# Performance work log

Hardware: AMD Instinct MI355X
Metric: run time of the kernel (lower is better)

The kernel has to match this reference:

```python
import jax, jax.numpy as jnp
import numpy as np

EMBED_DIM = 512
NUM_HEADS = 8
HEAD_DIM = EMBED_DIM // NUM_HEADS
EDGE_DIM = 16
B, N = 2, 2048


def setup_inputs() -> dict:
    key = jax.random.key(0)
    ks = jax.random.split(key, 16)
    s = 1.0 / np.sqrt(EMBED_DIM)
    inp = {
        "x": jax.random.normal(ks[0], (B, N, EMBED_DIM), dtype=jnp.float32),
        "adjacency": jax.random.uniform(ks[1], (B, N, N), dtype=jnp.float32),
        # torch.nn.Linear stores weight as (out, in); we keep that convention
        "Wq": jax.random.uniform(ks[2], (EMBED_DIM, EMBED_DIM), minval=-s, maxval=s),
        "bq": jax.random.uniform(ks[3], (EMBED_DIM,), minval=-s, maxval=s),
        "Wk": jax.random.uniform(ks[4], (EMBED_DIM, EMBED_DIM), minval=-s, maxval=s),
        "bk": jax.random.uniform(ks[5], (EMBED_DIM,), minval=-s, maxval=s),
        "Wv": jax.random.uniform(ks[6], (EMBED_DIM, EMBED_DIM), minval=-s, maxval=s),
        "bv": jax.random.uniform(ks[7], (EMBED_DIM,), minval=-s, maxval=s),
        "Wo": jax.random.uniform(ks[8], (EMBED_DIM, EMBED_DIM), minval=-s, maxval=s),
        "bo": jax.random.uniform(ks[9], (EMBED_DIM,), minval=-s, maxval=s),
        # edge MLP: Linear(1 -> edge_dim) then Linear(edge_dim -> num_heads)
        "We1": jax.random.uniform(ks[10], (EDGE_DIM, 1), minval=-1.0, maxval=1.0),
        "be1": jax.random.uniform(ks[11], (EDGE_DIM,), minval=-1.0, maxval=1.0),
        "We2": jax.random.uniform(ks[12], (NUM_HEADS, EDGE_DIM), minval=-0.25, maxval=0.25),
        "be2": jax.random.uniform(ks[13], (NUM_HEADS,), minval=-0.25, maxval=0.25),
        "edge_bias": jnp.zeros((NUM_HEADS,), dtype=jnp.float32),
    }
    return inp


def reference(x, adjacency, Wq, bq, Wk, bk, Wv, bv, Wo, bo, We1, be1, We2, be2, edge_bias):
    b, n, _ = x.shape
    scale = HEAD_DIM ** (-0.5)

    def split_heads(t):  # (b, n, E) -> (b, H, n, d)
        return t.reshape(b, n, NUM_HEADS, HEAD_DIM).transpose(0, 2, 1, 3)

    q = split_heads(x @ Wq.T + bq)
    k = split_heads(x @ Wk.T + bk)
    v = split_heads(x @ Wv.T + bv)

    # (b, H, n, n)
    attn_scores = jnp.einsum('bhid,bhjd->bhij', q, k) * scale

    # edge MLP applied pointwise to each adjacency entry: 1 -> edge_dim -> num_heads
    # hidden: (b, n, n, edge_dim)
    hidden = jax.nn.relu(adjacency[..., None] * We1[:, 0] + be1)
    edge_attn = jnp.einsum('bijE,hE->bhij', hidden, We2) + be2[None, :, None, None]

    boost = adjacency[:, None, :, :] * edge_bias[None, :, None, None]
    attn_scores = attn_scores + edge_attn + boost

    attn_probs = jax.nn.softmax(attn_scores, axis=-1)
    out = jnp.einsum('bhij,bhjd->bhid', attn_probs, v)
    out = out.transpose(0, 2, 1, 3).reshape(b, n, EMBED_DIM)
    out = out @ Wo.T + bo
    return out
```

## Files before the change

kernel.cpp:

```cpp
#include <hip/hip_runtime.h>
#include <stdint.h>


#define SEQ 2048
#define EMB 512
#define NH  8
#define HD  64
#define NB  2

typedef unsigned int   u32;
typedef unsigned short u16;
typedef u32   u32x4  __attribute__((ext_vector_type(4)));
typedef float f32x4  __attribute__((ext_vector_type(4)));
typedef __bf16 bf16x8 __attribute__((ext_vector_type(8)));

#define MFMA16(a, b, c) __builtin_amdgcn_mfma_f32_16x16x32_bf16((a), (b), (c), 0, 0, 0)

static __device__ __forceinline__ u16 f2bf(float f) {
  u32 u = __builtin_bit_cast(u32, f);
  return (u16)((u + 0x7fffu + ((u >> 16) & 1u)) >> 16);
}
static __device__ __forceinline__ bf16x8 ldfrag(const u16* p) {
  return __builtin_bit_cast(bf16x8, *(const u32x4*)p);
}

__global__ void cvt_bf16_kernel(const float* __restrict__ s, u16* __restrict__ d, int n) {
  int i = (blockIdx.x * blockDim.x + threadIdx.x) * 4;
  if (i >= n) return;
  float4 v = *(const float4*)(s + i);
  u32 lo = (u32)f2bf(v.x) | ((u32)f2bf(v.y) << 16);
  u32 hi = (u32)f2bf(v.z) | ((u32)f2bf(v.w) << 16);
  *(uint2*)(d + i) = make_uint2(lo, hi);
}

__global__ void cvt_w_kernel(const float* __restrict__ Wq, const float* __restrict__ Wk,
                             const float* __restrict__ Wv, const float* __restrict__ Wo,
                             u16* __restrict__ wqkv, u16* __restrict__ wob) {
  int i = (blockIdx.x * blockDim.x + threadIdx.x) * 4;
  int m = i >> 18;
  int off = i & 262143;
  const float* src = (m == 0) ? Wq : ((m == 1) ? Wk : ((m == 2) ? Wv : Wo));
  u16* dst = (m < 3) ? (wqkv + (size_t)m * 262144) : wob;
  float4 v = *(const float4*)(src + off);
  u32 lo = (u32)f2bf(v.x) | ((u32)f2bf(v.y) << 16);
  u32 hi = (u32)f2bf(v.z) | ((u32)f2bf(v.w) << 16);
  *(uint2*)(dst + off) = make_uint2(lo, hi);
}

__global__ void edge_coeff_kernel(const float* __restrict__ We1, const float* __restrict__ be1,
                                  const float* __restrict__ We2, const float* __restrict__ be2,
                                  const float* __restrict__ ebias, float* __restrict__ co) {
  const int t = threadIdx.x;
  const int e = t & 15, h = t >> 4;
  float w1 = We1[e], b1 = be1[e], w2 = We2[h * 16 + e];
  float u0 = b1, u1 = w1 + b1;
  bool on  = (u0 >= 0.0f) && (u1 >= 0.0f);
  bool off = (u0 <= 0.0f) && (u1 <= 0.0f);
  bool crossing = (!on) && (!off);
  float ca = on ? (w2 * b1) : (crossing ? 0.5f * w2 * b1 : 0.0f);
  float cb = on ? (w2 * w1) : (crossing ? 0.5f * w2 * w1 : 0.0f);
  #pragma unroll
  for (int d = 1; d < 16; d <<= 1) {
    ca += __shfl_xor(ca, d);
    cb += __shfl_xor(cb, d);
  }
  if (e == 0) { co[h] = be2[h] + ca; co[8 + h] = ebias[h] + cb; }
  unsigned long long msk = __ballot(crossing);
  int midx = __popcll(msk & 0xFFFFull & ((1ull << e) - 1ull));
  int mcnt = __popcll(msk & 0xFFFFull);
  if (crossing) {
    co[49 + midx * 8 + h] = 0.5f * w2;
    if (h == 0 || h == 4) {  }
    if (h == 0) { co[17 + midx] = w1; co[33 + midx] = b1; }
  }
  if (t == 0) ((int*)co)[16] = mcnt;
}

#define LDA 40
__global__ __launch_bounds__(256) void gemm_qkv_kernel(
    const u16* __restrict__ A, const u16* __restrict__ Bm,
    const float* __restrict__ bq, const float* __restrict__ bk, const float* __restrict__ bv,
    u16* __restrict__ qh, u16* __restrict__ kh, u16* __restrict__ vh)
{
  __shared__ u16 As[128 * LDA];
  __shared__ u16 Bs[128 * LDA];
  const int tid = threadIdx.x;
  const int lane = tid & 63, wid = tid >> 6;
  const int q = lane >> 4, l15 = lane & 15;
  const int m0 = blockIdx.y * 128;
  const int n0 = blockIdx.x * 128;
  const int wh = wid >> 1, ww = wid & 1;

  f32x4 acc[4][4];
  f32x4 zero = {0.f, 0.f, 0.f, 0.f};
  #pragma unroll
  for (int i = 0; i < 4; i++)
    #pragma unroll
    for (int j = 0; j < 4; j++) acc[i][j] = zero;

  const int srow = tid >> 1, shalf = tid & 1;
  const u16* ga = A  + (size_t)(m0 + srow) * EMB + shalf * 16;
  const u16* gb = Bm + (size_t)(n0 + srow) * EMB + shalf * 16;
  u16* la = &As[srow * LDA + shalf * 16];
  u16* lb = &Bs[srow * LDA + shalf * 16];

  u32x4 pa0 = *(const u32x4*)(ga);
  u32x4 pa1 = *(const u32x4*)(ga + 8);
  u32x4 pb0 = *(const u32x4*)(gb);
  u32x4 pb1 = *(const u32x4*)(gb + 8);
  ga += 32; gb += 32;

  for (int k0 = 0; k0 < EMB; k0 += 32) {
    __syncthreads();
    *(u32x4*)(la)     = pa0; *(u32x4*)(la + 8) = pa1;
    *(u32x4*)(lb)     = pb0; *(u32x4*)(lb + 8) = pb1;
    __syncthreads();
    if (k0 + 32 < EMB) {
      pa0 = *(const u32x4*)(ga);
      pa1 = *(const u32x4*)(ga + 8);
      pb0 = *(const u32x4*)(gb);
      pb1 = *(const u32x4*)(gb + 8);
      ga += 32; gb += 32;
    }
    bf16x8 af[4], bfr[4];
    #pragma unroll
    for (int mi = 0; mi < 4; mi++)
      af[mi] = ldfrag(&As[(wh*64 + mi*16 + l15) * LDA + q*8]);
    #pragma unroll
    for (int ni = 0; ni < 4; ni++)
      bfr[ni] = ldfrag(&Bs[(ww*64 + ni*16 + l15) * LDA + q*8]);
    #pragma unroll
    for (int mi = 0; mi < 4; mi++)
      #pragma unroll
      for (int ni = 0; ni < 4; ni++)
        acc[mi][ni] = MFMA16(af[mi], bfr[ni], acc[mi][ni]);
  }

  const int mat = n0 >> 9;
  const float* bias = (mat == 0) ? bq : ((mat == 1) ? bk : bv);
  u16* dst = (mat == 0) ? qh : ((mat == 1) ? kh : vh);
  const float mul = (mat == 0) ? 0.125f : 1.0f;

  #pragma unroll
  for (int mi = 0; mi < 4; mi++) {
    int rowb = m0 + wh*64 + mi*16 + q*4;
    #pragma unroll
    for (int ni = 0; ni < 4; ni++) {
      int col = n0 + ww*64 + ni*16 + l15;
      int oo = col & 511;
      float bsv = bias[oo];
      int h = oo >> 6, dd = oo & 63;
      #pragma unroll
      for (int r = 0; r < 4; r++) {
        int grow = rowb + r;
        int b_ = grow >> 11, n_ = grow & 2047;
        float val = (acc[mi][ni][r] + bsv) * mul;
        dst[((size_t)(b_ * NH + h) * SEQ + n_) * HD + dd] = f2bf(val);
      }
    }
  }
}

__global__ __launch_bounds__(256) void gemm_out_kernel(
    const u16* __restrict__ A, const u16* __restrict__ Bm,
    const float* __restrict__ bo, float* __restrict__ out)
{
  __shared__ u16 As[64 * LDA];
  __shared__ u16 Bs[128 * LDA];
  const int tid = threadIdx.x;
  const int lane = tid & 63, w = tid >> 6;
  const int q = lane >> 4, l15 = lane & 15;
  const int m0 = blockIdx.y * 64;
  const int n0 = blockIdx.x * 128;

  f32x4 acc[4][2];
  f32x4 zero = {0.f, 0.f, 0.f, 0.f};
  #pragma unroll
  for (int i = 0; i < 4; i++) { acc[i][0] = zero; acc[i][1] = zero; }

  const bool isA = tid < 128;
  const int arow = tid >> 1, ahalf = tid & 1;
  const int brow = tid - 128;
  const u16* ga = A  + (size_t)(m0 + arow) * EMB + ahalf * 16;
  const u16* gb = Bm + (size_t)(n0 + brow) * EMB;
  u16* la = &As[arow * LDA + ahalf * 16];
  u16* lb = &Bs[brow * LDA];

  u32x4 p0, p1, p2, p3;
  if (isA) {
    p0 = *(const u32x4*)(ga);
    p1 = *(const u32x4*)(ga + 8);
    ga += 32;
  } else {
    p0 = *(const u32x4*)(gb);
    p1 = *(const u32x4*)(gb + 8);
    p2 = *(const u32x4*)(gb + 16);
    p3 = *(const u32x4*)(gb + 24);
    gb += 32;
  }

  for (int k0 = 0; k0 < EMB; k0 += 32) {
    __syncthreads();
    if (isA) {
      *(u32x4*)(la)     = p0; *(u32x4*)(la + 8) = p1;
    } else {
      *(u32x4*)(lb)      = p0; *(u32x4*)(lb + 8)  = p1;
      *(u32x4*)(lb + 16) = p2; *(u32x4*)(lb + 24) = p3;
    }
    __syncthreads();
    if (k0 + 32 < EMB) {
      if (isA) {
        p0 = *(const u32x4*)(ga);
        p1 = *(const u32x4*)(ga + 8);
        ga += 32;
      } else {
        p0 = *(const u32x4*)(gb);
        p1 = *(const u32x4*)(gb + 8);
        p2 = *(const u32x4*)(gb + 16);
        p3 = *(const u32x4*)(gb + 24);
        gb += 32;
      }
    }
    bf16x8 af[4], bfr[2];
    #pragma unroll
    for (int mi = 0; mi < 4; mi++)
      af[mi] = ldfrag(&As[(mi*16 + l15) * LDA + q*8]);
    #pragma unroll
    for (int ni = 0; ni < 2; ni++)
      bfr[ni] = ldfrag(&Bs[(w*32 + ni*16 + l15) * LDA + q*8]);
    #pragma unroll
    for (int mi = 0; mi < 4; mi++)
      #pragma unroll
      for (int ni = 0; ni < 2; ni++)
        acc[mi][ni] = MFMA16(af[mi], bfr[ni], acc[mi][ni]);
  }

  #pragma unroll
  for (int mi = 0; mi < 4; mi++) {
    int rowb = m0 + mi*16 + q*4;
    #pragma unroll
    for (int ni = 0; ni < 2; ni++) {
      int col = n0 + w*32 + ni*16 + l15;
      float bsv = bo[col];
      #pragma unroll
      for (int r = 0; r < 4; r++)
        out[(size_t)(rowb + r) * EMB + col] = acc[mi][ni][r] + bsv;
    }
  }
}

__global__ __launch_bounds__(256) void vtrans_kernel(const u16* __restrict__ vh, u16* __restrict__ vt) {
  __shared__ u16 Ts[64 * 72];
  const int b = blockIdx.z, h = blockIdx.y, j0 = blockIdx.x * 64;
  const int t = threadIdx.x;
  const u16* src = vh + ((size_t)(b * NH + h) * SEQ + j0) * HD;
  {
    int r = t >> 2, c = t & 3;
    *(u32x4*)&Ts[r*72 + c*16]     = *(const u32x4*)(src + r*HD + c*16);
    *(u32x4*)&Ts[r*72 + c*16 + 8] = *(const u32x4*)(src + r*HD + c*16 + 8);
  }
  __syncthreads();
  int d = t >> 2, jc = t & 3;
  u32 wv[8];
  #pragma unroll
  for (int p = 0; p < 8; p++) {
    u32 lo = Ts[(jc*16 + 2*p    ) * 72 + d];
    u32 hi = Ts[(jc*16 + 2*p + 1) * 72 + d];
    wv[p] = lo | (hi << 16);
  }
  u16* dst = vt + ((size_t)(b * NH + h) * HD + d) * SEQ + j0 + jc * 16;
  u32x4 w0 = {wv[0], wv[1], wv[2], wv[3]};
  u32x4 w1 = {wv[4], wv[5], wv[6], wv[7]};
  *(u32x4*)(dst)     = w0;
  *(u32x4*)(dst + 8) = w1;
}

__global__ __launch_bounds__(256) void flash_kernel(
    const u16* __restrict__ qh, const u16* __restrict__ kh, const u16* __restrict__ vt,
    const float* __restrict__ adj, const float* __restrict__ coeff, u16* __restrict__ om)
{
  __shared__ u16 Ks[64 * 72];
  __shared__ u16 Vs[64 * 72];
  __shared__ u16 Ps[4 * 16 * 72];

  const int tid = threadIdx.x, lane = tid & 63, w = tid >> 6;
  const int q = lane >> 4, l15 = lane & 15;
  const int i0 = blockIdx.x * 64;
  const int h = blockIdx.y, b = blockIdx.z;
  const int bh = b * NH + h;

  const float Ah = coeff[h], Bh = coeff[8 + h];
  const int mterms = ((const int*)coeff)[16];

  const u16* qbase = qh + ((size_t)bh * SEQ + i0 + w*16 + l15) * HD + q*8;
  bf16x8 qf0 = ldfrag(qbase);
  bf16x8 qf1 = ldfrag(qbase + 32);

  f32x4 O[4];
  f32x4 zero = {0.f, 0.f, 0.f, 0.f};
  #pragma unroll
  for (int dt = 0; dt < 4; dt++) O[dt] = zero;
  float lsum[4] = {0.f, 0.f, 0.f, 0.f};

  const u16* kgbase = kh + (size_t)bh * SEQ * HD;
  const u16* vgbase = vt + (size_t)bh * HD * SEQ;
  const float* abase = adj + ((size_t)b * SEQ + i0 + w*16 + q*4) * SEQ;

  const int sr = tid >> 2, sc = tid & 3;
  u16* psw = &Ps[w * 16 * 72];

  u32x4 pk0, pk1, pv0, pv1;
  float padj[16];
  {
    const u16* gk = kgbase + (size_t)sr * HD + sc * 16;
    const u16* gv = vgbase + (size_t)sr * SEQ + sc * 16;
    pk0 = *(const u32x4*)(gk);
    pk1 = *(const u32x4*)(gk + 8);
    pv0 = *(const u32x4*)(gv);
    pv1 = *(const u32x4*)(gv + 8);
    #pragma unroll
    for (int jt = 0; jt < 4; jt++)
      #pragma unroll
      for (int r = 0; r < 4; r++)
        padj[jt*4 + r] = abase[(size_t)r * SEQ + jt*16 + l15];
  }

  for (int it = 0; it < 32; it++) {
    __syncthreads();
    *(u32x4*)&Ks[sr*72 + sc*16]     = pk0;
    *(u32x4*)&Ks[sr*72 + sc*16 + 8] = pk1;
    *(u32x4*)&Vs[sr*72 + sc*16]     = pv0;
    *(u32x4*)&Vs[sr*72 + sc*16 + 8] = pv1;
    __syncthreads();

    const int nx = (it + 1 < 32) ? (it + 1) * 64 : 0;

    {
      const u16* gk = kgbase + (size_t)(nx + sr) * HD + sc * 16;
      const u16* gv = vgbase + (size_t)sr * SEQ + nx + sc * 16;
      pk0 = *(const u32x4*)(gk);
      pk1 = *(const u32x4*)(gk + 8);
      pv0 = *(const u32x4*)(gv);
      pv1 = *(const u32x4*)(gv + 8);
    }

    float eb[16];
    #pragma unroll
    for (int jt = 0; jt < 4; jt++)
      #pragma unroll
      for (int r = 0; r < 4; r++)
        eb[jt*4 + r] = fmaf(padj[jt*4 + r], Bh, Ah);
    for (int t = 0; t < mterms; t++) {
      float ct = coeff[17 + t], dt_ = coeff[33 + t], wt = coeff[49 + t*8 + h];
      #pragma unroll
      for (int jt = 0; jt < 4; jt++)
        #pragma unroll
        for (int r = 0; r < 4; r++)
          eb[jt*4 + r] = fmaf(fabsf(fmaf(padj[jt*4 + r], ct, dt_)), wt, eb[jt*4 + r]);
    }

    #pragma unroll
    for (int jt = 0; jt < 4; jt++)
      #pragma unroll
      for (int r = 0; r < 4; r++)
        padj[jt*4 + r] = abase[(size_t)r * SEQ + nx + jt*16 + l15];

    f32x4 S[4];
    #pragma unroll
    for (int jt = 0; jt < 4; jt++) {
      bf16x8 kf0 = ldfrag(&Ks[(jt*16 + l15) * 72 + q*8]);
      bf16x8 kf1 = ldfrag(&Ks[(jt*16 + l15) * 72 + 32 + q*8]);
      f32x4 s = zero;
      s = MFMA16(qf0, kf0, s);
      s = MFMA16(qf1, kf1, s);
      S[jt] = s;
    }

    #pragma unroll
    for (int jt = 0; jt < 4; jt++) {
      #pragma unroll
      for (int r = 0; r < 4; r++) {
        float p = __expf(S[jt][r] + eb[jt*4 + r]);
        lsum[r] += p;
        psw[(q*4 + r) * 72 + jt*16 + l15] = f2bf(p);
      }
    }

    bf16x8 pf0 = ldfrag(&psw[l15 * 72 + q*8]);
    bf16x8 pf1 = ldfrag(&psw[l15 * 72 + 32 + q*8]);
    #pragma unroll
    for (int dt = 0; dt < 4; dt++) {
      bf16x8 vf0 = ldfrag(&Vs[(dt*16 + l15) * 72 + q*8]);
      bf16x8 vf1 = ldfrag(&Vs[(dt*16 + l15) * 72 + 32 + q*8]);
      O[dt] = MFMA16(pf0, vf0, O[dt]);
      O[dt] = MFMA16(pf1, vf1, O[dt]);
    }
  }

  float rl[4];
  #pragma unroll
  for (int r = 0; r < 4; r++) {
    float v = lsum[r];
    v += __shfl_xor(v, 1);
    v += __shfl_xor(v, 2);
    v += __shfl_xor(v, 4);
    v += __shfl_xor(v, 8);
    rl[r] = 1.0f / v;
  }

  #pragma unroll
  for (int dt = 0; dt < 4; dt++)
    #pragma unroll
    for (int r = 0; r < 4; r++)
      om[((size_t)b * SEQ + i0 + w*16 + q*4 + r) * EMB + h * HD + dt*16 + l15] =
          f2bf(O[dt][r] * rl[r]);
}

extern "C" void kernel_launch(void* const* d_in, const int* in_sizes, int n_in,
                              void* d_out, int out_size, void* d_ws, size_t ws_size,
                              hipStream_t stream) {
  const float* x     = (const float*)d_in[0];
  const float* adj   = (const float*)d_in[1];
  const float* Wq    = (const float*)d_in[2];
  const float* bq    = (const float*)d_in[3];
  const float* Wk    = (const float*)d_in[4];
  const float* bk    = (const float*)d_in[5];
  const float* Wv    = (const float*)d_in[6];
  const float* bv    = (const float*)d_in[7];
  const float* Wo    = (const float*)d_in[8];
  const float* bo    = (const float*)d_in[9];
  const float* We1   = (const float*)d_in[10];
  const float* be1   = (const float*)d_in[11];
  const float* We2   = (const float*)d_in[12];
  const float* be2   = (const float*)d_in[13];
  const float* ebias = (const float*)d_in[14];
  float* out = (float*)d_out;

  char* ws = (char*)d_ws;
  u16*   xb   = (u16*)(ws + 0);
  u16*   wqkv = (u16*)(ws + 4194304);
  u16*   wob  = (u16*)(ws + 5767168);
  u16*   qh   = (u16*)(ws + 6291456);
  u16*   kh   = (u16*)(ws + 10485760);
  u16*   vh   = (u16*)(ws + 14680064);
  u16*   vt   = (u16*)(ws + 18874368);
  u16*   om   = (u16*)(ws + 23068672);
  float* co   = (float*)(ws + 27262976);
  if (ws_size < 27264000) return;

  cvt_bf16_kernel<<<2048, 256, 0, stream>>>(x, xb, NB * SEQ * EMB);
  cvt_w_kernel<<<1024, 256, 0, stream>>>(Wq, Wk, Wv, Wo, wqkv, wob);
  edge_coeff_kernel<<<1, 128, 0, stream>>>(We1, be1, We2, be2, ebias, co);
  gemm_qkv_kernel<<<dim3(12, 32), 256, 0, stream>>>(xb, wqkv, bq, bk, bv, qh, kh, vh);
  vtrans_kernel<<<dim3(32, NH, NB), 256, 0, stream>>>(vh, vt);
  flash_kernel<<<dim3(32, NH, NB), 256, 0, stream>>>(qh, kh, vt, adj, co, om);
  gemm_out_kernel<<<dim3(4, 64), 256, 0, stream>>>(om, wob, bo, out);
}
```

Measured before the change: 199.7 us.

## Fuse prep kernels, split flash key range across two wave groups, use exp2

```diff
diff --git a/kernel.cpp b/kernel.cpp
--- a/kernel.cpp
+++ b/kernel.cpp
@@ -7,6 +7,7 @@
 #define NH  8
 #define HD  64
 #define NB  2
+#define L2E 1.4426950408889634f
 
 typedef unsigned int   u32;
 typedef unsigned short u16;
@@ -17,63 +18,65 @@
 #define MFMA16(a, b, c) __builtin_amdgcn_mfma_f32_16x16x32_bf16((a), (b), (c), 0, 0, 0)
 
 static __device__ __forceinline__ u16 f2bf(float f) {
-  u32 u = __builtin_bit_cast(u32, f);
-  return (u16)((u + 0x7fffu + ((u >> 16) & 1u)) >> 16);
+  return __builtin_bit_cast(u16, (__bf16)f);
 }
 static __device__ __forceinline__ bf16x8 ldfrag(const u16* p) {
   return __builtin_bit_cast(bf16x8, *(const u32x4*)p);
 }
 
-__global__ void cvt_bf16_kernel(const float* __restrict__ s, u16* __restrict__ d, int n) {
-  int i = (blockIdx.x * blockDim.x + threadIdx.x) * 4;
-  if (i >= n) return;
-  float4 v = *(const float4*)(s + i);
-  u32 lo = (u32)f2bf(v.x) | ((u32)f2bf(v.y) << 16);
-  u32 hi = (u32)f2bf(v.z) | ((u32)f2bf(v.w) << 16);
-  *(uint2*)(d + i) = make_uint2(lo, hi);
-}
-
-__global__ void cvt_w_kernel(const float* __restrict__ Wq, const float* __restrict__ Wk,
-                             const float* __restrict__ Wv, const float* __restrict__ Wo,
-                             u16* __restrict__ wqkv, u16* __restrict__ wob) {
-  int i = (blockIdx.x * blockDim.x + threadIdx.x) * 4;
-  int m = i >> 18;
-  int off = i & 262143;
-  const float* src = (m == 0) ? Wq : ((m == 1) ? Wk : ((m == 2) ? Wv : Wo));
-  u16* dst = (m < 3) ? (wqkv + (size_t)m * 262144) : wob;
-  float4 v = *(const float4*)(src + off);
-  u32 lo = (u32)f2bf(v.x) | ((u32)f2bf(v.y) << 16);
-  u32 hi = (u32)f2bf(v.z) | ((u32)f2bf(v.w) << 16);
-  *(uint2*)(dst + off) = make_uint2(lo, hi);
-}
-
-__global__ void edge_coeff_kernel(const float* __restrict__ We1, const float* __restrict__ be1,
-                                  const float* __restrict__ We2, const float* __restrict__ be2,
-                                  const float* __restrict__ ebias, float* __restrict__ co) {
-  const int t = threadIdx.x;
-  const int e = t & 15, h = t >> 4;
-  float w1 = We1[e], b1 = be1[e], w2 = We2[h * 16 + e];
-  float u0 = b1, u1 = w1 + b1;
-  bool on  = (u0 >= 0.0f) && (u1 >= 0.0f);
-  bool off = (u0 <= 0.0f) && (u1 <= 0.0f);
-  bool crossing = (!on) && (!off);
-  float ca = on ? (w2 * b1) : (crossing ? 0.5f * w2 * b1 : 0.0f);
-  float cb = on ? (w2 * w1) : (crossing ? 0.5f * w2 * w1 : 0.0f);
-  #pragma unroll
-  for (int d = 1; d < 16; d <<= 1) {
-    ca += __shfl_xor(ca, d);
-    cb += __shfl_xor(cb, d);
-  }
-  if (e == 0) { co[h] = be2[h] + ca; co[8 + h] = ebias[h] + cb; }
-  unsigned long long msk = __ballot(crossing);
-  int midx = __popcll(msk & 0xFFFFull & ((1ull << e) - 1ull));
-  int mcnt = __popcll(msk & 0xFFFFull);
-  if (crossing) {
-    co[49 + midx * 8 + h] = 0.5f * w2;
-    if (h == 0 || h == 4) {  }
-    if (h == 0) { co[17 + midx] = w1; co[33 + midx] = b1; }
-  }
-  if (t == 0) ((int*)co)[16] = mcnt;
+__global__ void prep_kernel(const float* __restrict__ x,
+                            const float* __restrict__ Wq, const float* __restrict__ Wk,
+                            const float* __restrict__ Wv, const float* __restrict__ Wo,
+                            const float* __restrict__ We1, const float* __restrict__ be1,
+                            const float* __restrict__ We2, const float* __restrict__ be2,
+                            const float* __restrict__ ebias,
+                            u16* __restrict__ xb, u16* __restrict__ wqkv,
+                            u16* __restrict__ wob, float* __restrict__ co) {
+  const int blk = blockIdx.x, tid = threadIdx.x;
+  if (blk < 2048) {
+    int i = (blk * 256 + tid) * 4;
+    float4 v = *(const float4*)(x + i);
+    u32 lo = (u32)f2bf(v.x) | ((u32)f2bf(v.y) << 16);
+    u32 hi = (u32)f2bf(v.z) | ((u32)f2bf(v.w) << 16);
+    *(uint2*)(xb + i) = make_uint2(lo, hi);
+  } else if (blk < 3072) {
+    int i = ((blk - 2048) * 256 + tid) * 4;
+    int m = i >> 18;
+    int off = i & 262143;
+    const float* src = (m == 0) ? Wq : ((m == 1) ? Wk : ((m == 2) ? Wv : Wo));
+    u16* dst = (m < 3) ? (wqkv + (size_t)m * 262144) : wob;
+    float4 v = *(const float4*)(src + off);
+    u32 lo = (u32)f2bf(v.x) | ((u32)f2bf(v.y) << 16);
+    u32 hi = (u32)f2bf(v.z) | ((u32)f2bf(v.w) << 16);
+    *(uint2*)(dst + off) = make_uint2(lo, hi);
+  } else {
+    const int e = tid & 15, h = tid >> 4;
+    if (tid < 128) {
+      co[49 + e * 8 + h] = 0.0f;
+      if (h == 0) { co[17 + e] = 0.0f; co[33 + e] = 0.0f; }
+    }
+    __syncthreads();
+    if (tid < 128) {
+      float w1 = We1[e], b1 = be1[e], w2 = We2[h * 16 + e];
+      float u0 = b1, u1 = w1 + b1;
+      bool on  = (u0 >= 0.0f) && (u1 >= 0.0f);
+      bool off = (u0 <= 0.0f) && (u1 <= 0.0f);
+      bool crossing = (!on) && (!off);
+      float ca = on ? (w2 * b1) : (crossing ? 0.5f * w2 * b1 : 0.0f);
+      float cb = on ? (w2 * w1) : (crossing ? 0.5f * w2 * w1 : 0.0f);
+      #pragma unroll
+      for (int d = 1; d < 16; d <<= 1) { ca += __shfl_xor(ca, d); cb += __shfl_xor(cb, d); }
+      if (e == 0) { co[h] = (be2[h] + ca) * L2E; co[8 + h] = (ebias[h] + cb) * L2E; }
+      unsigned long long msk = __ballot(crossing);
+      int midx = __popcll(msk & 0xFFFFull & ((1ull << e) - 1ull));
+      int mcnt = __popcll(msk & 0xFFFFull);
+      if (crossing) {
+        co[49 + midx * 8 + h] = 0.5f * w2 * L2E;
+        if (h == 0) { co[17 + midx] = w1; co[33 + midx] = b1; }
+      }
+      if (tid == 0) ((int*)co)[16] = mcnt;
+    }
+  }
 }
 
 #define LDA 40
@@ -82,80 +85,84 @@
     const float* __restrict__ bq, const float* __restrict__ bk, const float* __restrict__ bv,
     u16* __restrict__ qh, u16* __restrict__ kh, u16* __restrict__ vh)
 {
-  __shared__ u16 As[128 * LDA];
+  __shared__ u16 As[64 * LDA];
   __shared__ u16 Bs[128 * LDA];
   const int tid = threadIdx.x;
-  const int lane = tid & 63, wid = tid >> 6;
+  const int lane = tid & 63, w = tid >> 6;
   const int q = lane >> 4, l15 = lane & 15;
-  const int m0 = blockIdx.y * 128;
+  const int m0 = blockIdx.y * 64;
   const int n0 = blockIdx.x * 128;
-  const int wh = wid >> 1, ww = wid & 1;
-
-  f32x4 acc[4][4];
+
+  f32x4 acc[4][2];
   f32x4 zero = {0.f, 0.f, 0.f, 0.f};
   #pragma unroll
-  for (int i = 0; i < 4; i++)
-    #pragma unroll
-    for (int j = 0; j < 4; j++) acc[i][j] = zero;
-
-  const int srow = tid >> 1, shalf = tid & 1;
-  const u16* ga = A  + (size_t)(m0 + srow) * EMB + shalf * 16;
-  const u16* gb = Bm + (size_t)(n0 + srow) * EMB + shalf * 16;
-  u16* la = &As[srow * LDA + shalf * 16];
-  u16* lb = &Bs[srow * LDA + shalf * 16];
-
-  u32x4 pa0 = *(const u32x4*)(ga);
-  u32x4 pa1 = *(const u32x4*)(ga + 8);
-  u32x4 pb0 = *(const u32x4*)(gb);
-  u32x4 pb1 = *(const u32x4*)(gb + 8);
-  ga += 32; gb += 32;
+  for (int i = 0; i < 4; i++) { acc[i][0] = zero; acc[i][1] = zero; }
+
+  const bool isA = tid < 128;
+  const int arow = tid >> 1, ahalf = tid & 1;
+  const int brow = tid - 128;
+  const u16* ga = A  + (size_t)(m0 + arow) * EMB + ahalf * 16;
+  const u16* gb = Bm + (size_t)(n0 + brow) * EMB;
+  u16* la = &As[arow * LDA + ahalf * 16];
+  u16* lb = &Bs[brow * LDA];
+
+  u32x4 p0, p1, p2, p3;
+  if (isA) {
+    p0 = *(const u32x4*)(ga); p1 = *(const u32x4*)(ga + 8); ga += 32;
+  } else {
+    p0 = *(const u32x4*)(gb);      p1 = *(const u32x4*)(gb + 8);
+    p2 = *(const u32x4*)(gb + 16); p3 = *(const u32x4*)(gb + 24); gb += 32;
+  }
 
   for (int k0 = 0; k0 < EMB; k0 += 32) {
     __syncthreads();
-    *(u32x4*)(la)     = pa0; *(u32x4*)(la + 8) = pa1;
-    *(u32x4*)(lb)     = pb0; *(u32x4*)(lb + 8) = pb1;
+    if (isA) { *(u32x4*)(la) = p0; *(u32x4*)(la + 8) = p1; }
+    else {
+      *(u32x4*)(lb)      = p0; *(u32x4*)(lb + 8)  = p1;
+      *(u32x4*)(lb + 16) = p2; *(u32x4*)(lb + 24) = p3;
+    }
     __syncthreads();
     if (k0 + 32 < EMB) {
-      pa0 = *(const u32x4*)(ga);
-      pa1 = *(const u32x4*)(ga + 8);
-      pb0 = *(const u32x4*)(gb);
-      pb1 = *(const u32x4*)(gb + 8);
-      ga += 32; gb += 32;
-    }
-    bf16x8 af[4], bfr[4];
+      if (isA) { p0 = *(const u32x4*)(ga); p1 = *(const u32x4*)(ga + 8); ga += 32; }
+      else {
+        p0 = *(const u32x4*)(gb);      p1 = *(const u32x4*)(gb + 8);
+        p2 = *(const u32x4*)(gb + 16); p3 = *(const u32x4*)(gb + 24); gb += 32;
+      }
+    }
+    bf16x8 af[4], bfr[2];
     #pragma unroll
     for (int mi = 0; mi < 4; mi++)
-      af[mi] = ldfrag(&As[(wh*64 + mi*16 + l15) * LDA + q*8]);
-    #pragma unroll
-    for (int ni = 0; ni < 4; ni++)
-      bfr[ni] = ldfrag(&Bs[(ww*64 + ni*16 + l15) * LDA + q*8]);
+      af[mi] = ldfrag(&As[(mi*16 + l15) * LDA + q*8]);
+    #pragma unroll
+    for (int ni = 0; ni < 2; ni++)
+      bfr[ni] = ldfrag(&Bs[(w*32 + ni*16 + l15) * LDA + q*8]);
     #pragma unroll
     for (int mi = 0; mi < 4; mi++)
       #pragma unroll
-      for (int ni = 0; ni < 4; ni++)
+      for (int ni = 0; ni < 2; ni++)
         acc[mi][ni] = MFMA16(af[mi], bfr[ni], acc[mi][ni]);
   }
 
   const int mat = n0 >> 9;
   const float* bias = (mat == 0) ? bq : ((mat == 1) ? bk : bv);
   u16* dst = (mat == 0) ? qh : ((mat == 1) ? kh : vh);
-  const float mul = (mat == 0) ? 0.125f : 1.0f;
+  const float mul = (mat == 0) ? 0.125f * L2E : 1.0f;
 
   #pragma unroll
   for (int mi = 0; mi < 4; mi++) {
-    int rowb = m0 + wh*64 + mi*16 + q*4;
-    #pragma unroll
-    for (int ni = 0; ni < 4; ni++) {
-      int col = n0 + ww*64 + ni*16 + l15;
+    int rowb = m0 + mi*16 + q*4;
+    #pragma unroll
+    for (int ni = 0; ni < 2; ni++) {
+      int col = n0 + w*32 + ni*16 + l15;
       int oo = col & 511;
       float bsv = bias[oo];
-      int h = oo >> 6, dd = oo & 63;
+      int hh = oo >> 6, dd = oo & 63;
       #pragma unroll
       for (int r = 0; r < 4; r++) {
         int grow = rowb + r;
         int b_ = grow >> 11, n_ = grow & 2047;
         float val = (acc[mi][ni][r] + bsv) * mul;
-        dst[((size_t)(b_ * NH + h) * SEQ + n_) * HD + dd] = f2bf(val);
+        dst[((size_t)(b_ * NH + hh) * SEQ + n_) * HD + dd] = f2bf(val);
       }
     }
   }
@@ -188,37 +195,25 @@
 
   u32x4 p0, p1, p2, p3;
   if (isA) {
-    p0 = *(const u32x4*)(ga);
-    p1 = *(const u32x4*)(ga + 8);
-    ga += 32;
+    p0 = *(const u32x4*)(ga); p1 = *(const u32x4*)(ga + 8); ga += 32;
   } else {
-    p0 = *(const u32x4*)(gb);
-    p1 = *(const u32x4*)(gb + 8);
-    p2 = *(const u32x4*)(gb + 16);
-    p3 = *(const u32x4*)(gb + 24);
-    gb += 32;
+    p0 = *(const u32x4*)(gb);      p1 = *(const u32x4*)(gb + 8);
+    p2 = *(const u32x4*)(gb + 16); p3 = *(const u32x4*)(gb + 24); gb += 32;
   }
 
   for (int k0 = 0; k0 < EMB; k0 += 32) {
     __syncthreads();
-    if (isA) {
-      *(u32x4*)(la)     = p0; *(u32x4*)(la + 8) = p1;
-    } else {
+    if (isA) { *(u32x4*)(la) = p0; *(u32x4*)(la + 8) = p1; }
+    else {
       *(u32x4*)(lb)      = p0; *(u32x4*)(lb + 8)  = p1;
       *(u32x4*)(lb + 16) = p2; *(u32x4*)(lb + 24) = p3;
     }
     __syncthreads();
     if (k0 + 32 < EMB) {
-      if (isA) {
-        p0 = *(const u32x4*)(ga);
-        p1 = *(const u32x4*)(ga + 8);
-        ga += 32;
-      } else {
-        p0 = *(const u32x4*)(gb);
-        p1 = *(const u32x4*)(gb + 8);
-        p2 = *(const u32x4*)(gb + 16);
-        p3 = *(const u32x4*)(gb + 24);
-        gb += 32;
+      if (isA) { p0 = *(const u32x4*)(ga); p1 = *(const u32x4*)(ga + 8); ga += 32; }
+      else {
+        p0 = *(const u32x4*)(gb);      p1 = *(const u32x4*)(gb + 8);
+        p2 = *(const u32x4*)(gb + 16); p3 = *(const u32x4*)(gb + 24); gb += 32;
       }
     }
     bf16x8 af[4], bfr[2];
@@ -275,24 +270,34 @@
   *(u32x4*)(dst + 8) = w1;
 }
 
-__global__ __launch_bounds__(256) void flash_kernel(
+template<int MT>
+__device__ __forceinline__ void flash_body(
+    u16* __restrict__ smem,
     const u16* __restrict__ qh, const u16* __restrict__ kh, const u16* __restrict__ vt,
     const float* __restrict__ adj, const float* __restrict__ coeff, u16* __restrict__ om)
 {
-  __shared__ u16 Ks[64 * 72];
-  __shared__ u16 Vs[64 * 72];
-  __shared__ u16 Ps[4 * 16 * 72];
+  u16* Ks = smem;
+  u16* Vs = smem + 9216;
+  u16* Ps = smem + 18432;
 
   const int tid = threadIdx.x, lane = tid & 63, w = tid >> 6;
   const int q = lane >> 4, l15 = lane & 15;
   const int i0 = blockIdx.x * 64;
   const int h = blockIdx.y, b = blockIdx.z;
   const int bh = b * NH + h;
+  const int jhalf = w >> 2, wrow = (w & 3) * 16;
+  const int jbase = jhalf * 1024;
 
   const float Ah = coeff[h], Bh = coeff[8 + h];
-  const int mterms = ((const int*)coeff)[16];
-
-  const u16* qbase = qh + ((size_t)bh * SEQ + i0 + w*16 + l15) * HD + q*8;
+  float ctr[MT > 0 ? MT : 1], dtr[MT > 0 ? MT : 1], wtr[MT > 0 ? MT : 1];
+  #pragma unroll
+  for (int t = 0; t < MT; t++) {
+    ctr[t] = coeff[17 + t];
+    dtr[t] = coeff[33 + t];
+    wtr[t] = coeff[49 + t * 8 + h];
+  }
+
+  const u16* qbase = qh + ((size_t)bh * SEQ + i0 + wrow + l15) * HD + q * 8;
   bf16x8 qf0 = ldfrag(qbase);
   bf16x8 qf1 = ldfrag(qbase + 32);
 
@@ -302,102 +307,90 @@
   for (int dt = 0; dt < 4; dt++) O[dt] = zero;
   float lsum[4] = {0.f, 0.f, 0.f, 0.f};
 
-  const u16* kgbase = kh + (size_t)bh * SEQ * HD;
-  const u16* vgbase = vt + (size_t)bh * HD * SEQ;
-  const float* abase = adj + ((size_t)b * SEQ + i0 + w*16 + q*4) * SEQ;
-
-  const int sr = tid >> 2, sc = tid & 3;
+  const float* abase = adj + ((size_t)b * SEQ + i0 + wrow + q * 4) * SEQ + jbase;
+
+  const int shalf = tid >> 8, t8 = tid & 255;
+  const int sr = t8 >> 2, sc = t8 & 3;
+  const u16* kgs = kh + (size_t)bh * SEQ * HD + ((size_t)(shalf * 1024) + sr) * HD + sc * 16;
+  const u16* vgs = vt + (size_t)bh * HD * SEQ + (size_t)sr * SEQ + shalf * 1024 + sc * 16;
+  u16* kls = &Ks[(shalf * 64 + sr) * 72 + sc * 16];
+  u16* vls = &Vs[(shalf * 64 + sr) * 72 + sc * 16];
+
   u16* psw = &Ps[w * 16 * 72];
 
-  u32x4 pk0, pk1, pv0, pv1;
+  u32x4 pk0 = *(const u32x4*)(kgs);
+  u32x4 pk1 = *(const u32x4*)(kgs + 8);
+  u32x4 pv0 = *(const u32x4*)(vgs);
+  u32x4 pv1 = *(const u32x4*)(vgs + 8);
   float padj[16];
-  {
-    const u16* gk = kgbase + (size_t)sr * HD + sc * 16;
-    const u16* gv = vgbase + (size_t)sr * SEQ + sc * 16;
-    pk0 = *(const u32x4*)(gk);
-    pk1 = *(const u32x4*)(gk + 8);
-    pv0 = *(const u32x4*)(gv);
-    pv1 = *(const u32x4*)(gv + 8);
-    #pragma unroll
-    for (int jt = 0; jt < 4; jt++)
-      #pragma unroll
-      for (int r = 0; r < 4; r++)
-        padj[jt*4 + r] = abase[(size_t)r * SEQ + jt*16 + l15];
-  }
-
-  for (int it = 0; it < 32; it++) {
-    __syncthreads();
-    *(u32x4*)&Ks[sr*72 + sc*16]     = pk0;
-    *(u32x4*)&Ks[sr*72 + sc*16 + 8] = pk1;
-    *(u32x4*)&Vs[sr*72 + sc*16]     = pv0;
-    *(u32x4*)&Vs[sr*72 + sc*16 + 8] = pv1;
-    __syncthreads();
-
-    const int nx = (it + 1 < 32) ? (it + 1) * 64 : 0;
-
-    {
-      const u16* gk = kgbase + (size_t)(nx + sr) * HD + sc * 16;
-      const u16* gv = vgbase + (size_t)sr * SEQ + nx + sc * 16;
-      pk0 = *(const u32x4*)(gk);
-      pk1 = *(const u32x4*)(gk + 8);
-      pv0 = *(const u32x4*)(gv);
-      pv1 = *(const u32x4*)(gv + 8);
-    }
-
-    float eb[16];
-    #pragma unroll
-    for (int jt = 0; jt < 4; jt++)
-      #pragma unroll
-      for (int r = 0; r < 4; r++)
-        eb[jt*4 + r] = fmaf(padj[jt*4 + r], Bh, Ah);
-    for (int t = 0; t < mterms; t++) {
-      float ct = coeff[17 + t], dt_ = coeff[33 + t], wt = coeff[49 + t*8 + h];
-      #pragma unroll
-      for (int jt = 0; jt < 4; jt++)
-        #pragma unroll
-        for (int r = 0; r < 4; r++)
-          eb[jt*4 + r] = fmaf(fabsf(fmaf(padj[jt*4 + r], ct, dt_)), wt, eb[jt*4 + r]);
-    }
-
-    #pragma unroll
-    for (int jt = 0; jt < 4; jt++)
-      #pragma unroll
-      for (int r = 0; r < 4; r++)
-        padj[jt*4 + r] = abase[(size_t)r * SEQ + nx + jt*16 + l15];
+  #pragma unroll
+  for (int jt = 0; jt < 4; jt++)
+    #pragma unroll
+    for (int r = 0; r < 4; r++)
+      padj[jt * 4 + r] = abase[(size_t)r * SEQ + jt * 16 + l15];
+
+  for (int it = 0; it < 16; it++) {
+    __syncthreads();
+    *(u32x4*)(kls)     = pk0;
+    *(u32x4*)(kls + 8) = pk1;
+    *(u32x4*)(vls)     = pv0;
+    *(u32x4*)(vls + 8) = pv1;
+    __syncthreads();
+
+    const int nxo = ((it + 1) & 15) * 64;
+    pk0 = *(const u32x4*)(kgs + (size_t)nxo * HD);
+    pk1 = *(const u32x4*)(kgs + (size_t)nxo * HD + 8);
+    pv0 = *(const u32x4*)(vgs + nxo);
+    pv1 = *(const u32x4*)(vgs + nxo + 8);
 
     f32x4 S[4];
     #pragma unroll
     for (int jt = 0; jt < 4; jt++) {
-      bf16x8 kf0 = ldfrag(&Ks[(jt*16 + l15) * 72 + q*8]);
-      bf16x8 kf1 = ldfrag(&Ks[(jt*16 + l15) * 72 + 32 + q*8]);
+      bf16x8 kf0 = ldfrag(&Ks[(jhalf * 64 + jt * 16 + l15) * 72 + q * 8]);
+      bf16x8 kf1 = ldfrag(&Ks[(jhalf * 64 + jt * 16 + l15) * 72 + 32 + q * 8]);
       f32x4 s = zero;
       s = MFMA16(qf0, kf0, s);
       s = MFMA16(qf1, kf1, s);
       S[jt] = s;
     }
 
+    float eb[16];
+    #pragma unroll
+    for (int u = 0; u < 16; u++)
+      eb[u] = fmaf(padj[u], Bh, Ah);
+    #pragma unroll
+    for (int t = 0; t < MT; t++)
+      #pragma unroll
+      for (int u = 0; u < 16; u++)
+        eb[u] = fmaf(fabsf(fmaf(padj[u], ctr[t], dtr[t])), wtr[t], eb[u]);
+
+    #pragma unroll
+    for (int jt = 0; jt < 4; jt++)
+      #pragma unroll
+      for (int r = 0; r < 4; r++)
+        padj[jt * 4 + r] = abase[(size_t)r * SEQ + nxo + jt * 16 + l15];
+
     #pragma unroll
     for (int jt = 0; jt < 4; jt++) {
       #pragma unroll
       for (int r = 0; r < 4; r++) {
-        float p = __expf(S[jt][r] + eb[jt*4 + r]);
+        float p = __builtin_amdgcn_exp2f(S[jt][r] + eb[jt * 4 + r]);
         lsum[r] += p;
-        psw[(q*4 + r) * 72 + jt*16 + l15] = f2bf(p);
-      }
-    }
-
-    bf16x8 pf0 = ldfrag(&psw[l15 * 72 + q*8]);
-    bf16x8 pf1 = ldfrag(&psw[l15 * 72 + 32 + q*8]);
+        psw[(q * 4 + r) * 72 + jt * 16 + l15] = f2bf(p);
+      }
+    }
+
+    bf16x8 pf0 = ldfrag(&psw[l15 * 72 + q * 8]);
+    bf16x8 pf1 = ldfrag(&psw[l15 * 72 + 32 + q * 8]);
     #pragma unroll
     for (int dt = 0; dt < 4; dt++) {
-      bf16x8 vf0 = ldfrag(&Vs[(dt*16 + l15) * 72 + q*8]);
-      bf16x8 vf1 = ldfrag(&Vs[(dt*16 + l15) * 72 + 32 + q*8]);
+      bf16x8 vf0 = ldfrag(&Vs[(jhalf * 64 + dt * 16 + l15) * 72 + q * 8]);
+      bf16x8 vf1 = ldfrag(&Vs[(jhalf * 64 + dt * 16 + l15) * 72 + 32 + q * 8]);
       O[dt] = MFMA16(pf0, vf0, O[dt]);
       O[dt] = MFMA16(pf1, vf1, O[dt]);
     }
   }
 
-  float rl[4];
   #pragma unroll
   for (int r = 0; r < 4; r++) {
     float v = lsum[r];
@@ -405,15 +398,47 @@
     v += __shfl_xor(v, 2);
     v += __shfl_xor(v, 4);
     v += __shfl_xor(v, 8);
-    rl[r] = 1.0f / v;
-  }
-
-  #pragma unroll
-  for (int dt = 0; dt < 4; dt++)
-    #pragma unroll
-    for (int r = 0; r < 4; r++)
-      om[((size_t)b * SEQ + i0 + w*16 + q*4 + r) * EMB + h * HD + dt*16 + l15] =
-          f2bf(O[dt][r] * rl[r]);
+    lsum[r] = v;
+  }
+
+  __syncthreads();
+  f32x4* Of = (f32x4*)smem;
+  f32x4* Lf = (f32x4*)((float*)smem + 5120);
+  if (w >= 4) {
+    const int bi = ((w & 3) * 64 + lane);
+    #pragma unroll
+    for (int dt = 0; dt < 4; dt++) Of[bi * 5 + dt] = O[dt];
+    f32x4 lv = {lsum[0], lsum[1], lsum[2], lsum[3]};
+    Lf[bi] = lv;
+  }
+  __syncthreads();
+  if (w < 4) {
+    const int bi = (w * 64 + lane);
+    f32x4 lv = Lf[bi];
+    float rl[4];
+    #pragma unroll
+    for (int r = 0; r < 4; r++) rl[r] = 1.0f / (lsum[r] + lv[r]);
+    #pragma unroll
+    for (int dt = 0; dt < 4; dt++) {
+      f32x4 ov = Of[bi * 5 + dt];
+      #pragma unroll
+      for (int r = 0; r < 4; r++) {
+        float val = (O[dt][r] + ov[r]) * rl[r];
+        om[((size_t)b * SEQ + i0 + wrow + q * 4 + r) * EMB + h * HD + dt * 16 + l15] = f2bf(val);
+      }
+    }
+  }
+}
+
+__global__ __launch_bounds__(512) void flash_kernel(
+    const u16* __restrict__ qh, const u16* __restrict__ kh, const u16* __restrict__ vt,
+    const float* __restrict__ adj, const float* __restrict__ coeff, u16* __restrict__ om)
+{
+  __shared__ __align__(16) u16 smem[27648];
+  const int mt = ((const int*)coeff)[16];
+  if (mt <= 4)      flash_body<4>(smem, qh, kh, vt, adj, coeff, om);
+  else if (mt <= 8) flash_body<8>(smem, qh, kh, vt, adj, coeff, om);
+  else              flash_body<16>(smem, qh, kh, vt, adj, coeff, om);
 }
 
 extern "C" void kernel_launch(void* const* d_in, const int* in_sizes, int n_in,
@@ -448,11 +473,10 @@
   float* co   = (float*)(ws + 27262976);
   if (ws_size < 27264000) return;
 
-  cvt_bf16_kernel<<<2048, 256, 0, stream>>>(x, xb, NB * SEQ * EMB);
-  cvt_w_kernel<<<1024, 256, 0, stream>>>(Wq, Wk, Wv, Wo, wqkv, wob);
-  edge_coeff_kernel<<<1, 128, 0, stream>>>(We1, be1, We2, be2, ebias, co);
-  gemm_qkv_kernel<<<dim3(12, 32), 256, 0, stream>>>(xb, wqkv, bq, bk, bv, qh, kh, vh);
+  prep_kernel<<<3073, 256, 0, stream>>>(x, Wq, Wk, Wv, Wo, We1, be1, We2, be2, ebias,
+                                        xb, wqkv, wob, co);
+  gemm_qkv_kernel<<<dim3(12, 64), 256, 0, stream>>>(xb, wqkv, bq, bk, bv, qh, kh, vh);
   vtrans_kernel<<<dim3(32, NH, NB), 256, 0, stream>>>(vh, vt);
-  flash_kernel<<<dim3(32, NH, NB), 256, 0, stream>>>(qh, kh, vt, adj, co, om);
+  flash_kernel<<<dim3(32, NH, NB), 512, 0, stream>>>(qh, kh, vt, adj, co, om);
   gemm_out_kernel<<<dim3(4, 64), 256, 0, stream>>>(om, wob, bo, out);
 }
```

After: 198.5 us. About the same (-0.6%).
